# Kernel optimization log

Measured on AMD Instinct MI355X. Metric: run time of the kernel, lower is better.

The kernel has to match this reference:

```python
import jax, jax.numpy as jnp
import numpy as np

PATCH = 3
STYLE_STRIDE = 1
SYNTH_STRIDE = 1


def _extract_patches(img, p, stride):
    # img: [1, C, H, W] -> flattened patches [N, C*p*p], row-major over (i, j),
    # matching torch's patches_sampling (channel-major, then kh, kw within a patch).
    pat = jax.lax.conv_general_dilated_patches(img, (p, p), (stride, stride), 'VALID')
    # pat: [1, C*p*p, oh, ow] with feature ordering (C, kh, kw)
    _, cpp, oh, ow = pat.shape
    return jnp.transpose(pat, (0, 2, 3, 1)).reshape(oh * ow, cpp)


def setup_inputs() -> dict:
    key = jax.random.key(0)
    k1, k2 = jax.random.split(key)
    input = jax.random.normal(k1, (1, 256, 96, 96), dtype=jnp.float32)
    target = jax.random.normal(k2, (1, 256, 96, 96), dtype=jnp.float32)
    return {"input": input, "target": target}


def reference(input, target):
    # Style patches (constructor: patches_sampling(target) with mrf_style_stride)
    style = _extract_patches(target, PATCH, STYLE_STRIDE)      # [S, D]
    # Synthesis patches with mrf_synthesis_stride
    synth = _extract_patches(input, PATCH, SYNTH_STRIDE)       # [Q, D]

    # Per-style-patch L2 norm (cal_patches_norm)
    style_norm = jnp.sqrt(jnp.sum(style * style, axis=1))      # [S]

    # conv2d(input, style_patches, stride) == patch dot products: [Q, S]
    resp = jnp.einsum('qd,sd->qs', synth, style)
    resp = resp / style_norm[None, :]

    # argmax over style patches per synthesis location (nearest-neighbor retrieval)
    nn_idx = jnp.argmax(resp, axis=1)                          # [Q]

    # gathered MSE: mean over patch elems, summed over Q, divided by Q -> mean
    diff = synth - style[nn_idx]                               # [Q, D]
    loss = jnp.mean(jnp.mean(diff * diff, axis=1))
    return loss
```

## Files before the change

### kernel.cpp

```cpp
#include <hip/hip_runtime.h>
#include <math.h>

#define NP 8836
#define PW 94
#define IW 96
#define CH 256
#define NTILE 70
#define KT2 18
#define NWG (NTILE * NTILE)
#define NPIX 9216
#define GTS 9216

typedef int   i32x4  __attribute__((ext_vector_type(4)));
typedef int   i32x8  __attribute__((ext_vector_type(8)));
typedef float f32x16 __attribute__((ext_vector_type(16)));

__device__ __forceinline__ unsigned int ordf(float f) {
  unsigned int u = __float_as_uint(f);
  return (u & 0x80000000u) ? ~u : (u | 0x80000000u);
}

__device__ __forceinline__ float blo(unsigned int x) {
  return __uint_as_float(x << 16);
}
__device__ __forceinline__ float bhi(unsigned int x) {
  return __uint_as_float(x & 0xFFFF0000u);
}

typedef const __attribute__((address_space(1))) void GvoidC;
typedef __attribute__((address_space(3))) void Lvoid;
__device__ __forceinline__ void gl16(const void* g, void* l) {
  __builtin_amdgcn_global_load_lds((GvoidC*)g, (Lvoid*)l, 16, 0, 0);
}

__global__ __launch_bounds__(256) void prep_kernel(
    const float* __restrict__ inA, const float* __restrict__ inB,
    unsigned int* __restrict__ TA, unsigned int* __restrict__ TB) {
  __shared__ float tile[64][65];
  int bid = blockIdx.x;
  const float* src; unsigned int* dst;
  if (bid < 576) { src = inA; dst = TA; }
  else           { src = inB; dst = TB; bid -= 576; }
  int cT  = bid & 3;
  int xyT = bid >> 2;
  int t = threadIdx.x;
  int l = t & 63, h = t >> 6;

  #pragma unroll
  for (int i = 0; i < 16; ++i) {
    int c = h * 16 + i;
    tile[c][l] = src[(size_t)(cT * 64 + c) * (IW * IW) + xyT * 64 + l];
  }
  __syncthreads();
  int cu = t & 15;
  #pragma unroll
  for (int i = 0; i < 4; ++i) {
    int xy = (t >> 4) + i * 16;
    int c = cu * 4;
    unsigned int v = __builtin_amdgcn_cvt_pk_fp8_f32(tile[c][xy],     tile[c + 1][xy], 0, false);
    v              = __builtin_amdgcn_cvt_pk_fp8_f32(tile[c + 2][xy], tile[c + 3][xy], v, true);
    dst[(size_t)(xyT * 64 + xy) * 64 + cT * 16 + cu] = v;
  }
}

__global__ void norms_kernel(const unsigned int* __restrict__ TA, const unsigned int* __restrict__ TB,
                             float* __restrict__ rnormS, float* __restrict__ normS,
                             float* __restrict__ normsqS, float* __restrict__ synsq) {
  int wid  = blockIdx.x * 4 + (threadIdx.x >> 6);
  int lane = threadIdx.x & 63;
  bool isStyle = wid < NP;
  int p = isStyle ? wid : wid - NP;
  if (p >= NP) return;
  const unsigned int* T = isStyle ? TB : TA;
  int pi = p / PW, pj = p % PW;
  float s = 0.f;
  #pragma unroll
  for (int kh = 0; kh < 3; ++kh) {
    #pragma unroll
    for (int kw = 0; kw < 3; ++kw) {
      unsigned int v = T[(size_t)((pi + kh) * IW + (pj + kw)) * 64 + lane];
      float f0 = __builtin_amdgcn_cvt_f32_fp8(v, 0);
      float f1 = __builtin_amdgcn_cvt_f32_fp8(v, 1);
      float f2 = __builtin_amdgcn_cvt_f32_fp8(v, 2);
      float f3 = __builtin_amdgcn_cvt_f32_fp8(v, 3);
      s += f0 * f0 + f1 * f1 + f2 * f2 + f3 * f3;
    }
  }
  #pragma unroll
  for (int m = 32; m >= 1; m >>= 1) s += __shfl_xor(s, m, 64);
  if (lane == 0) {
    if (isStyle) {
      normsqS[p] = s;
      float n = sqrtf(s);
      normS[p]  = n;
      rnormS[p] = 1.f / n;
    } else {
      synsq[p] = s;
    }
  }
}

__device__ __forceinline__ i32x8 ldfrag(const unsigned char* rowp, int o0, int o1) {
  i32x4 lo = *(const i32x4*)(rowp + o0);
  i32x4 hi = *(const i32x4*)(rowp + o1);
  return __builtin_shufflevector(lo, hi, 0, 1, 2, 3, 4, 5, 6, 7);
}

__global__ __launch_bounds__(256, 2) void g_gemm_kernel(
    const unsigned char* __restrict__ TA, const unsigned char* __restrict__ TB,
    unsigned short* __restrict__ GT) {
  __shared__ unsigned char As[128 * 128];
  __shared__ unsigned char Bs[128 * 128];

  int orig = blockIdx.x;
  int pid = (orig & 7) * 648 + (orig >> 3);
  int yt = pid % 72, xt = pid / 72;
  int y0 = yt * 128, x0 = xt * 128;
  int t = threadIdx.x, lane = t & 63, wave = t >> 6;
  int wm = wave >> 1, wn = wave & 1;

  int rr = t >> 3;
  int qc = (t & 7) ^ (rr & 7);
  const unsigned char* gA[4];
  const unsigned char* gB[4];
  #pragma unroll
  for (int i = 0; i < 4; ++i) {
    gA[i] = TB + (size_t)(y0 + 32 * i + rr) * CH + qc * 16;
    gB[i] = TA + (size_t)(x0 + 32 * i + rr) * CH + qc * 16;
  }
  unsigned char* lA = As + t * 16;
  unsigned char* lB = Bs + t * 16;

  f32x16 acc[2][2];
  #pragma unroll
  for (int mi = 0; mi < 2; ++mi)
    #pragma unroll
    for (int ni = 0; ni < 2; ++ni)
      #pragma unroll
      for (int j = 0; j < 16; ++j) acc[mi][ni][j] = 0.f;

  int kq = lane >> 5, sw = lane & 7;
  const unsigned char* Arow = As + (size_t)(wm * 64 + (lane & 31)) * 128;
  const unsigned char* Brow = Bs + (size_t)(wn * 64 + (lane & 31)) * 128;

  #pragma unroll 1
  for (int kt = 0; kt < 2; ++kt) {
    int choff = kt * 128;
    if (kt) __syncthreads();
    #pragma unroll
    for (int i = 0; i < 4; ++i) {
      gl16(gA[i] + choff, lA + i * 4096);
      gl16(gB[i] + choff, lB + i * 4096);
    }
    __syncthreads();
    #pragma unroll
    for (int h = 0; h < 2; ++h) {
      int c0 = 2 * kq + 4 * h;
      int o0 = (c0 ^ sw) * 16, o1 = ((c0 + 1) ^ sw) * 16;
      i32x8 af[2], bf[2];
      #pragma unroll
      for (int mi = 0; mi < 2; ++mi) af[mi] = ldfrag(Arow + mi * 32 * 128, o0, o1);
      #pragma unroll
      for (int ni = 0; ni < 2; ++ni) bf[ni] = ldfrag(Brow + ni * 32 * 128, o0, o1);
      #pragma unroll
      for (int mi = 0; mi < 2; ++mi)
        #pragma unroll
        for (int ni = 0; ni < 2; ++ni)
          acc[mi][ni] = __builtin_amdgcn_mfma_scale_f32_32x32x64_f8f6f4(
              af[mi], bf[ni], acc[mi][ni],
              0, 0, 0, 0x7F7F7F7F, 0, 0x7F7F7F7F);
    }
  }

  int col = lane & 31, half = lane >> 5;
  #pragma unroll
  for (int mi = 0; mi < 2; ++mi) {
    #pragma unroll
    for (int ni = 0; ni < 2; ++ni) {
      size_t ybase = (size_t)(y0 + wm * 64 + mi * 32 + 4 * half);
      size_t xg    = (size_t)(x0 + wn * 64 + ni * 32 + col);
      unsigned short* p = GT + ybase * GTS + xg;
      #pragma unroll
      for (int g = 0; g < 4; ++g)
        #pragma unroll
        for (int j = 0; j < 4; ++j) {
          unsigned int u = __float_as_uint(acc[mi][ni][4 * g + j]);
          unsigned short b = (unsigned short)((u + 0x7FFFu + ((u >> 16) & 1u)) >> 16);
          p[(size_t)(j + 8 * g) * GTS] = b;
        }
    }
  }
}

__global__ __launch_bounds__(256) void tapsum_kernel(
    const unsigned short* __restrict__ GT, const float* __restrict__ rnormS,
    unsigned long long* __restrict__ best) {
  __shared__ unsigned long long sm[4][96];
  int orig = blockIdx.x;
  int xcd = orig & 7, idx = orig >> 3;
  int pid = (xcd < 4 ? xcd * 1105 : 4 * 1105 + (xcd - 4) * 1104) + idx;
  int d = pid / 94, pos = pid - d * 94;
  int qi = pos;
  int si = pos + d; if (si >= 94) si -= 94;

  int t = threadIdx.x;
  int sjg = t >> 6, l = t & 63;

  unsigned long long cand0 = 0ull, cand1 = 0ull;
  if (l < 48) {
    int lc = l < 47 ? l : 46;
    int sj0 = sjg * 12;
    int niter = (sjg == 3) ? 11 : 12;

    unsigned int off0 = (unsigned)(((si + 0) * 96 + sj0) * GTS + (qi + 0) * 96 + 2 * lc);
    unsigned int off1 = (unsigned)(((si + 1) * 96 + sj0) * GTS + (qi + 1) * 96 + 2 * lc);
    unsigned int off2 = (unsigned)(((si + 2) * 96 + sj0) * GTS + (qi + 2) * 96 + 2 * lc);

    const float* rnp = rnormS + si * 94 + sj0;
    float bv0 = -3.0e38f, bv1 = -3.0e38f;
    int bs0 = sj0, bs1 = sj0;
    for (int j = 0; j < niter; ++j) {
      unsigned int e0_0 = *(const unsigned int*)(GT + off0);
      unsigned int a_0  = *(const unsigned int*)(GT + off0 + GTS);
      unsigned int b_0  = *(const unsigned int*)(GT + off0 + GTS + 2);
      unsigned int c_0  = *(const unsigned int*)(GT + off0 + 2 * GTS + 2);
      unsigned int e0_1 = *(const unsigned int*)(GT + off1);
      unsigned int a_1  = *(const unsigned int*)(GT + off1 + GTS);
      unsigned int b_1  = *(const unsigned int*)(GT + off1 + GTS + 2);
      unsigned int c_1  = *(const unsigned int*)(GT + off1 + 2 * GTS + 2);
      unsigned int e0_2 = *(const unsigned int*)(GT + off2);
      unsigned int a_2  = *(const unsigned int*)(GT + off2 + GTS);
      unsigned int b_2  = *(const unsigned int*)(GT + off2 + GTS + 2);
      unsigned int c_2  = *(const unsigned int*)(GT + off2 + 2 * GTS + 2);
      float rn = rnp[j];

      float a0 = (((blo(e0_0) + blo(c_0)) + bhi(a_1)) + blo(e0_2)) + blo(c_2);
      float a1 = ((bhi(a_0) + blo(e0_1)) + blo(c_1)) + bhi(a_2);
      float v0 = (a0 + a1) * rn;
      float a0b = (((bhi(e0_0) + bhi(c_0)) + blo(b_1)) + bhi(e0_2)) + bhi(c_2);
      float a1b = ((blo(b_0) + bhi(e0_1)) + bhi(c_1)) + blo(b_2);
      float v1 = (a0b + a1b) * rn;

      int sj = sj0 + j;
      if (v0 > bv0) { bv0 = v0; bs0 = sj; }
      if (v1 > bv1) { bv1 = v1; bs1 = sj; }
      off0 += GTS; off1 += GTS; off2 += GTS;
    }
    if (2 * l < 94) {
      int s = si * 94 + bs0;
      cand0 = ((unsigned long long)ordf(bv0) << 32) |
              (unsigned long long)(0xFFFFFFFFu - (unsigned)s);
    }
    if (2 * l + 1 < 94) {
      int s = si * 94 + bs1;
      cand1 = ((unsigned long long)ordf(bv1) << 32) |
              (unsigned long long)(0xFFFFFFFFu - (unsigned)s);
    }
    sm[sjg][2 * l]     = cand0;
    sm[sjg][2 * l + 1] = cand1;
  }
  __syncthreads();
  if (t < 94) {
    unsigned long long c0 = sm[0][t], c1 = sm[1][t];
    unsigned long long c2 = sm[2][t], c3 = sm[3][t];
    unsigned long long ca = c0 > c1 ? c0 : c1;
    unsigned long long cb = c2 > c3 ? c2 : c3;
    unsigned long long c  = ca > cb ? ca : cb;
    atomicMax(best + (size_t)(qi * 94 + t) * 8, c);
  }
}

__global__ __launch_bounds__(256, 2) void gemm_argmax_kernel(
    const unsigned char* __restrict__ TA, const unsigned char* __restrict__ TB,
    const float* __restrict__ rnormS, unsigned long long* __restrict__ best) {
  __shared__ unsigned char As[128 * 128];
  __shared__ unsigned char Bs[128 * 128];

  int orig = blockIdx.x;
  int xcd = orig & 7, idx = orig >> 3;
  int pid = (xcd < 4 ? xcd * 613 : 4 * 613 + (xcd - 4) * 612) + idx;

  int mt = pid % NTILE, nt = pid / NTILE;
  int q0 = mt * 128, s0 = nt * 128;
  int t = threadIdx.x, lane = t & 63, wave = t >> 6;
  int wm = wave >> 1, wn = wave & 1;

  int rr = t >> 3;
  int qc = (t & 7) ^ (rr & 7);
  const unsigned char* gA[4];
  const unsigned char* gB[4];
  #pragma unroll
  for (int i = 0; i < 4; ++i) {
    int qa = q0 + 32 * i + rr; if (qa > NP - 1) qa = NP - 1;
    int sa = s0 + 32 * i + rr; if (sa > NP - 1) sa = NP - 1;
    gA[i] = TA + (size_t)((qa / PW) * IW + (qa % PW)) * CH + qc * 16;
    gB[i] = TB + (size_t)((sa / PW) * IW + (sa % PW)) * CH + qc * 16;
  }
  unsigned char* lA = As + t * 16;
  unsigned char* lB = Bs + t * 16;

  f32x16 acc[2][2];
  #pragma unroll
  for (int mi = 0; mi < 2; ++mi)
    #pragma unroll
    for (int ni = 0; ni < 2; ++ni)
      #pragma unroll
      for (int j = 0; j < 16; ++j) acc[mi][ni][j] = 0.f;

  int kq = lane >> 5, sw = lane & 7;
  const unsigned char* Arow = As + (size_t)(wm * 64 + (lane & 31)) * 128;
  const unsigned char* Brow = Bs + (size_t)(wn * 64 + (lane & 31)) * 128;

  #pragma unroll 1
  for (int kt = 0; kt < KT2; ++kt) {
    int chunk = kt >> 1;
    int kh = chunk / 3, kw = chunk - kh * 3;
    int choff = (kh * IW + kw) * CH + (kt & 1) * 128;
    if (kt) __syncthreads();
    #pragma unroll
    for (int i = 0; i < 4; ++i) {
      gl16(gA[i] + choff, lA + i * 4096);
      gl16(gB[i] + choff, lB + i * 4096);
    }
    __syncthreads();
    #pragma unroll
    for (int h = 0; h < 2; ++h) {
      int c0 = 2 * kq + 4 * h;
      int o0 = (c0 ^ sw) * 16, o1 = ((c0 + 1) ^ sw) * 16;
      i32x8 af[2], bf[2];
      #pragma unroll
      for (int mi = 0; mi < 2; ++mi) af[mi] = ldfrag(Arow + mi * 32 * 128, o0, o1);
      #pragma unroll
      for (int ni = 0; ni < 2; ++ni) bf[ni] = ldfrag(Brow + ni * 32 * 128, o0, o1);
      #pragma unroll
      for (int mi = 0; mi < 2; ++mi)
        #pragma unroll
        for (int ni = 0; ni < 2; ++ni)
          acc[mi][ni] = __builtin_amdgcn_mfma_scale_f32_32x32x64_f8f6f4(
              af[mi], bf[ni], acc[mi][ni],
              0, 0, 0, 0x7F7F7F7F, 0, 0x7F7F7F7F);
    }
  }

  int col = lane & 31, half = lane >> 5;
  float rn[2]; int sc[2]; bool sv[2];
  #pragma unroll
  for (int ni = 0; ni < 2; ++ni) {
    int s = s0 + wn * 64 + ni * 32 + col;
    sc[ni] = s;
    sv[ni] = (s < NP);
    rn[ni] = sv[ni] ? rnormS[s] : 0.f;
  }
  #pragma unroll
  for (int mi = 0; mi < 2; ++mi) {
    #pragma unroll
    for (int reg = 0; reg < 16; ++reg) {
      unsigned long long p = 0ull;
      #pragma unroll
      for (int ni = 0; ni < 2; ++ni) {
        float v = acc[mi][ni][reg] * rn[ni];
        unsigned long long cand =
            ((unsigned long long)ordf(v) << 32) |
            (unsigned long long)(0xFFFFFFFFu - (unsigned)sc[ni]);
        cand = sv[ni] ? cand : 0ull;
        if (cand > p) p = cand;
      }
      #pragma unroll
      for (int sh = 16; sh >= 1; sh >>= 1) {
        unsigned long long o = __shfl_xor(p, sh, 64);
        if (o > p) p = o;
      }
      int q = q0 + wm * 64 + mi * 32 + (reg & 3) + 8 * (reg >> 2) + 4 * half;
      if (col == 0 && q < NP) atomicMax(best + (size_t)q * 8, p);
    }
  }
}

__global__ void finalize_kernel(const unsigned long long* __restrict__ best,
                                const float* __restrict__ normS,
                                const float* __restrict__ normsqS,
                                const float* __restrict__ synsq,
                                float* __restrict__ out) {
  __shared__ float sm[256];
  int t = threadIdx.x;
  float accum = 0.f;
  for (int q = t; q < NP; q += 256) {
    unsigned long long p = best[(size_t)q * 8];
    unsigned int o   = (unsigned int)(p >> 32);
    unsigned int idx = 0xFFFFFFFFu - (unsigned int)(p & 0xFFFFFFFFull);
    unsigned int u   = (o & 0x80000000u) ? (o & 0x7FFFFFFFu) : ~o;
    float resp = __uint_as_float(u);
    float dot  = resp * normS[idx];
    accum += synsq[q] - 2.f * dot + normsqS[idx];
  }
  sm[t] = accum;
  __syncthreads();
  for (int s = 128; s >= 1; s >>= 1) {
    if (t < s) sm[t] += sm[t + s];
    __syncthreads();
  }
  if (t == 0) out[0] = sm[0] / ((float)NP * 2304.f);
}

extern "C" void kernel_launch(void* const* d_in, const int* in_sizes, int n_in,
                              void* d_out, int out_size, void* d_ws, size_t ws_size,
                              hipStream_t stream) {
  const float* inA = (const float*)d_in[0];
  const float* inB = (const float*)d_in[1];
  float* out = (float*)d_out;

  char* ws = (char*)d_ws;
  unsigned char* TA = (unsigned char*)ws;
  unsigned char* TB = (unsigned char*)(ws + 2359296);
  float* rnormS  = (float*)(ws + 4718592);
  float* normS   = (float*)(ws + 4718592 + 35344);
  float* normsqS = (float*)(ws + 4718592 + 70688);
  float* synsq   = (float*)(ws + 4718592 + 106032);
  unsigned long long* best = (unsigned long long*)(ws + 4718592 + 141376);
  const size_t GT_OFF = 4718592ull + 141376ull + 565504ull;
  unsigned short* GT = (unsigned short*)(ws + GT_OFF);
  const size_t NEED = GT_OFF + (size_t)NPIX * NPIX * 2;

  (void)hipMemsetAsync(best, 0, (size_t)NP * 64, stream);
  prep_kernel<<<dim3(1152), dim3(256), 0, stream>>>(inA, inB, (unsigned int*)TA, (unsigned int*)TB);
  norms_kernel<<<dim3((2 * NP + 3) / 4), dim3(256), 0, stream>>>(
      (const unsigned int*)TA, (const unsigned int*)TB, rnormS, normS, normsqS, synsq);
  if (ws_size >= NEED) {
    g_gemm_kernel<<<dim3(72 * 72), dim3(256), 0, stream>>>(TA, TB, GT);
    tapsum_kernel<<<dim3(NP), dim3(256), 0, stream>>>(GT, rnormS, best);
  } else {
    gemm_argmax_kernel<<<dim3(NWG), dim3(256), 0, stream>>>(TA, TB, rnormS, best);
  }
  finalize_kernel<<<dim3(1), dim3(256), 0, stream>>>(best, normS, normsqS, synsq, out);
}
```

Before: 216.6 us.

## Stage tapsum GT slab into LDS and parallelize finalize across blocks

The tapsum kernel now copies the three 96x96 bf16 GT blocks it needs into 54KB of shared memory with 16-byte async loads, then each wave scans 24 style columns reading from LDS instead of issuing strided global loads. This is meant to replace scattered, poorly coalesced global reads with one bulk coalesced copy, at the cost of high LDS use that limits occupancy. The finalize kernel is split across 35 blocks using wave shuffles and an atomicAdd into a zeroed output, replacing the single-block serial reduction. The atomic float add makes the summation order nondeterministic.

```diff
diff --git a/kernel.cpp b/kernel.cpp
--- a/kernel.cpp
+++ b/kernel.cpp
@@ -195,6 +195,7 @@
 __global__ __launch_bounds__(256) void tapsum_kernel(
     const unsigned short* __restrict__ GT, const float* __restrict__ rnormS,
     unsigned long long* __restrict__ best) {
+  __shared__ unsigned char glds[55296];
   __shared__ unsigned long long sm[4][96];
   int orig = blockIdx.x;
   int xcd = orig & 7, idx = orig >> 3;
@@ -204,60 +205,69 @@
   int si = pos + d; if (si >= 94) si -= 94;
 
   int t = threadIdx.x;
-  int sjg = t >> 6, l = t & 63;
+
+  const unsigned char* GTb = (const unsigned char*)GT;
+  for (int k = 0; k < 14; ++k) {
+    int c = k * 256 + t;
+    if (c < 3456) {
+      int b = c / 1152, rem = c - b * 1152;
+      int r = rem / 12, s = rem - r * 12;
+      size_t gaddr = ((size_t)((si + b) * 96 + r) * GTS + (size_t)(qi + b) * 96) * 2
+                     + (size_t)s * 16;
+      gl16(GTb + gaddr, glds + c * 16);
+    }
+  }
+  __syncthreads();
+
+  int w = t >> 6, l = t & 63;
+  int sj0 = w * 24;
+  int niter = (w == 3) ? 22 : 24;
 
   unsigned long long cand0 = 0ull, cand1 = 0ull;
-  if (l < 48) {
-    int lc = l < 47 ? l : 46;
-    int sj0 = sjg * 12;
-    int niter = (sjg == 3) ? 11 : 12;
-
-    unsigned int off0 = (unsigned)(((si + 0) * 96 + sj0) * GTS + (qi + 0) * 96 + 2 * lc);
-    unsigned int off1 = (unsigned)(((si + 1) * 96 + sj0) * GTS + (qi + 1) * 96 + 2 * lc);
-    unsigned int off2 = (unsigned)(((si + 2) * 96 + sj0) * GTS + (qi + 2) * 96 + 2 * lc);
-
+  if (l < 47) {
     const float* rnp = rnormS + si * 94 + sj0;
     float bv0 = -3.0e38f, bv1 = -3.0e38f;
     int bs0 = sj0, bs1 = sj0;
+    int va0 = sj0 * 192 + 4 * l;
+    int va1 = va0 + 18432;
+    int va2 = va0 + 36864;
     for (int j = 0; j < niter; ++j) {
-      unsigned int e0_0 = *(const unsigned int*)(GT + off0);
-      unsigned int a_0  = *(const unsigned int*)(GT + off0 + GTS);
-      unsigned int b_0  = *(const unsigned int*)(GT + off0 + GTS + 2);
-      unsigned int c_0  = *(const unsigned int*)(GT + off0 + 2 * GTS + 2);
-      unsigned int e0_1 = *(const unsigned int*)(GT + off1);
-      unsigned int a_1  = *(const unsigned int*)(GT + off1 + GTS);
-      unsigned int b_1  = *(const unsigned int*)(GT + off1 + GTS + 2);
-      unsigned int c_1  = *(const unsigned int*)(GT + off1 + 2 * GTS + 2);
-      unsigned int e0_2 = *(const unsigned int*)(GT + off2);
-      unsigned int a_2  = *(const unsigned int*)(GT + off2 + GTS);
-      unsigned int b_2  = *(const unsigned int*)(GT + off2 + GTS + 2);
-      unsigned int c_2  = *(const unsigned int*)(GT + off2 + 2 * GTS + 2);
+      unsigned int d00_0 = *(const unsigned int*)(glds + va0);
+      unsigned int d10_0 = *(const unsigned int*)(glds + va0 + 192);
+      unsigned int d11_0 = *(const unsigned int*)(glds + va0 + 196);
+      unsigned int d21_0 = *(const unsigned int*)(glds + va0 + 388);
+      unsigned int d00_1 = *(const unsigned int*)(glds + va1);
+      unsigned int d10_1 = *(const unsigned int*)(glds + va1 + 192);
+      unsigned int d11_1 = *(const unsigned int*)(glds + va1 + 196);
+      unsigned int d21_1 = *(const unsigned int*)(glds + va1 + 388);
+      unsigned int d00_2 = *(const unsigned int*)(glds + va2);
+      unsigned int d10_2 = *(const unsigned int*)(glds + va2 + 192);
+      unsigned int d11_2 = *(const unsigned int*)(glds + va2 + 196);
+      unsigned int d21_2 = *(const unsigned int*)(glds + va2 + 388);
       float rn = rnp[j];
 
-      float a0 = (((blo(e0_0) + blo(c_0)) + bhi(a_1)) + blo(e0_2)) + blo(c_2);
-      float a1 = ((bhi(a_0) + blo(e0_1)) + blo(c_1)) + bhi(a_2);
+      float a0 = (((blo(d00_0) + blo(d21_0)) + bhi(d10_1)) + blo(d00_2)) + blo(d21_2);
+      float a1 = ((bhi(d10_0) + blo(d00_1)) + blo(d21_1)) + bhi(d10_2);
       float v0 = (a0 + a1) * rn;
-      float a0b = (((bhi(e0_0) + bhi(c_0)) + blo(b_1)) + bhi(e0_2)) + bhi(c_2);
-      float a1b = ((blo(b_0) + bhi(e0_1)) + bhi(c_1)) + blo(b_2);
+      float a0b = (((bhi(d00_0) + bhi(d21_0)) + blo(d11_1)) + bhi(d00_2)) + bhi(d21_2);
+      float a1b = ((blo(d11_0) + bhi(d00_1)) + bhi(d21_1)) + blo(d11_2);
       float v1 = (a0b + a1b) * rn;
 
       int sj = sj0 + j;
       if (v0 > bv0) { bv0 = v0; bs0 = sj; }
       if (v1 > bv1) { bv1 = v1; bs1 = sj; }
-      off0 += GTS; off1 += GTS; off2 += GTS;
-    }
-    if (2 * l < 94) {
-      int s = si * 94 + bs0;
+      va0 += 192; va1 += 192; va2 += 192;
+    }
+    {
+      int s0i = si * 94 + bs0;
       cand0 = ((unsigned long long)ordf(bv0) << 32) |
-              (unsigned long long)(0xFFFFFFFFu - (unsigned)s);
-    }
-    if (2 * l + 1 < 94) {
-      int s = si * 94 + bs1;
+              (unsigned long long)(0xFFFFFFFFu - (unsigned)s0i);
+      int s1i = si * 94 + bs1;
       cand1 = ((unsigned long long)ordf(bv1) << 32) |
-              (unsigned long long)(0xFFFFFFFFu - (unsigned)s);
-    }
-    sm[sjg][2 * l]     = cand0;
-    sm[sjg][2 * l + 1] = cand1;
+              (unsigned long long)(0xFFFFFFFFu - (unsigned)s1i);
+    }
+    sm[w][2 * l]     = cand0;
+    sm[w][2 * l + 1] = cand1;
   }
   __syncthreads();
   if (t < 94) {
@@ -376,30 +386,30 @@
   }
 }
 
-__global__ void finalize_kernel(const unsigned long long* __restrict__ best,
-                                const float* __restrict__ normS,
-                                const float* __restrict__ normsqS,
-                                const float* __restrict__ synsq,
-                                float* __restrict__ out) {
-  __shared__ float sm[256];
+__global__ __launch_bounds__(256) void finalize_kernel(
+    const unsigned long long* __restrict__ best,
+    const float* __restrict__ normS,
+    const float* __restrict__ normsqS,
+    const float* __restrict__ synsq,
+    float* __restrict__ out) {
+  __shared__ float swv[4];
   int t = threadIdx.x;
-  float accum = 0.f;
-  for (int q = t; q < NP; q += 256) {
+  int q = blockIdx.x * 256 + t;
+  float a = 0.f;
+  if (q < NP) {
     unsigned long long p = best[(size_t)q * 8];
     unsigned int o   = (unsigned int)(p >> 32);
     unsigned int idx = 0xFFFFFFFFu - (unsigned int)(p & 0xFFFFFFFFull);
     unsigned int u   = (o & 0x80000000u) ? (o & 0x7FFFFFFFu) : ~o;
     float resp = __uint_as_float(u);
     float dot  = resp * normS[idx];
-    accum += synsq[q] - 2.f * dot + normsqS[idx];
-  }
-  sm[t] = accum;
+    a = (synsq[q] - 2.f * dot + normsqS[idx]) * (1.f / ((float)NP * 2304.f));
+  }
+  #pragma unroll
+  for (int m = 32; m >= 1; m >>= 1) a += __shfl_xor(a, m, 64);
+  if ((t & 63) == 0) swv[t >> 6] = a;
   __syncthreads();
-  for (int s = 128; s >= 1; s >>= 1) {
-    if (t < s) sm[t] += sm[t + s];
-    __syncthreads();
-  }
-  if (t == 0) out[0] = sm[0] / ((float)NP * 2304.f);
+  if (t == 0) atomicAdd(out, (swv[0] + swv[1]) + (swv[2] + swv[3]));
 }
 
 extern "C" void kernel_launch(void* const* d_in, const int* in_sizes, int n_in,
@@ -422,6 +432,7 @@
   const size_t NEED = GT_OFF + (size_t)NPIX * NPIX * 2;
 
   (void)hipMemsetAsync(best, 0, (size_t)NP * 64, stream);
+  (void)hipMemsetAsync(out, 0, sizeof(float), stream);
   prep_kernel<<<dim3(1152), dim3(256), 0, stream>>>(inA, inB, (unsigned int*)TA, (unsigned int*)TB);
   norms_kernel<<<dim3((2 * NP + 3) / 4), dim3(256), 0, stream>>>(
       (const unsigned int*)TA, (const unsigned int*)TB, rnormS, normS, normsqS, synsq);
@@ -431,5 +442,5 @@
   } else {
     gemm_argmax_kernel<<<dim3(NWG), dim3(256), 0, stream>>>(TA, TB, rnormS, best);
   }
-  finalize_kernel<<<dim3(1), dim3(256), 0, stream>>>(best, normS, normsqS, synsq, out);
-}
+  finalize_kernel<<<dim3(35), dim3(256), 0, stream>>>(best, normS, normsqS, synsq, out);
+}
```

Measured after the change: 229.2 us. 1.06x slower.
